# Kernel tuning notes

Hardware: AMD Instinct MI355X
Metric: run time of the kernel (lower is better)

## Reference

```python
import jax, jax.numpy as jnp
import numpy as np

B, T, C, K, NH, HID, L, NC = 16, 500, 512, 7, 8, 2048, 3, 2
HD = C // NH
SCALE = float(1.0 / np.sqrt(HD))


def setup_inputs() -> dict:
    key = jax.random.key(0)
    ks = jax.random.split(key, 24)
    rn = lambda k, sh, s=0.02: jax.random.normal(k, sh, jnp.float32) * s
    return {
        'x': jax.random.normal(ks[0], (B, T, C), jnp.float32),
        'dw_w': rn(ks[1], (L, NC, C, 1, K)),   # depthwise conv kernels (groups=C)
        'dw_b': rn(ks[2], (L, NC, C)),
        'pw_w': rn(ks[3], (L, NC, C, C)),       # pointwise 1x1 conv weights [out,in]
        'pw_b': rn(ks[4], (L, NC, C)),
        'cln_g': jnp.ones((L, NC, C), jnp.float32),
        'cln_b': jnp.zeros((L, NC, C), jnp.float32),
        'wq': rn(ks[5], (L, C, C)), 'bq': rn(ks[6], (L, C)),
        'wk': rn(ks[7], (L, C, C)), 'bk': rn(ks[8], (L, C)),
        'wv': rn(ks[9], (L, C, C)), 'bv': rn(ks[10], (L, C)),
        'wo': rn(ks[11], (L, C, C)), 'bo': rn(ks[12], (L, C)),
        'aln_g': jnp.ones((L, C), jnp.float32), 'aln_b': jnp.zeros((L, C), jnp.float32),
        'w1': rn(ks[13], (L, HID, C)), 'b1': rn(ks[14], (L, HID)),
        'w2': rn(ks[15], (L, C, HID)), 'b2': rn(ks[16], (L, C)),
        'fln_g': jnp.ones((L, C), jnp.float32), 'fln_b': jnp.zeros((L, C), jnp.float32),
    }


def _ln(x, g, b):
    m = x.mean(-1, keepdims=True)
    v = ((x - m) ** 2).mean(-1, keepdims=True)
    return (x - m) / jnp.sqrt(v + 1e-5) * g + b


def _conv_block(x, w, b, pw, pb, g, be):
    # x: (B, C, T). Depthwise conv (groups=C), padding K//2 keeps T.
    out = jax.lax.conv_general_dilated(
        x, w, window_strides=(1,), padding=[(K // 2, K // 2)],
        feature_group_count=C, dimension_numbers=('NCH', 'OIH', 'NCH')) + b[None, :, None]
    out = jnp.einsum('bct,oc->bot', out, pw) + pb[None, :, None]  # pointwise 1x1
    out = _ln(out.transpose(0, 2, 1), g, be).transpose(0, 2, 1)
    return out


def _attn(x, wq, bq, wk, bk, wv, bv, wo, bo):
    Bx, Tx, Cx = x.shape
    def split(h):
        return h.reshape(Bx, Tx, NH, HD).transpose(0, 2, 1, 3)  # (B,H,T,HD)
    q = split(x @ wq.T + bq)
    k = split(x @ wk.T + bk)
    v = split(x @ wv.T + bv)
    att = jnp.einsum('bhqd,bhkd->bhqk', q, k) * SCALE
    mask = jnp.tril(jnp.ones((Tx, Tx), bool))
    att = jnp.where(mask, att, -1e10)
    att = jax.nn.softmax(att, axis=-1)
    y = jnp.einsum('bhqk,bhkd->bhqd', att, v)
    y = y.transpose(0, 2, 1, 3).reshape(Bx, Tx, Cx)
    return y @ wo.T + bo


def _block(x, l, dw_w, dw_b, pw_w, pw_b, cln_g, cln_b, wq, bq, wk, bk, wv, bv,
           wo, bo, aln_g, aln_b, w1, b1, w2, b2, fln_g, fln_b):
    out = x.transpose(0, 2, 1)  # (B, C, T)
    for c in range(NC):
        out = _conv_block(out, dw_w[l, c], dw_b[l, c], pw_w[l, c], pw_b[l, c],
                          cln_g[l, c], cln_b[l, c])
    out = out.transpose(0, 2, 1)  # (B, T, C)
    out = _attn(out, wq[l], bq[l], wk[l], bk[l], wv[l], bv[l], wo[l], bo[l])
    out = _ln(out, aln_g[l], aln_b[l])
    out = _ln(jax.nn.relu(out @ w1[l].T + b1[l]) @ w2[l].T + b2[l], fln_g[l], fln_b[l])
    return out  # eval mode: dropouts are identity


def reference(x, dw_w, dw_b, pw_w, pw_b, cln_g, cln_b, wq, bq, wk, bk, wv, bv,
              wo, bo, aln_g, aln_b, w1, b1, w2, b2, fln_g, fln_b):
    outs = []
    h = x
    for l in range(L):
        h = _block(h, l, dw_w, dw_b, pw_w, pw_b, cln_g, cln_b, wq, bq, wk, bk,
                   wv, bv, wo, bo, aln_g, aln_b, w1, b1, w2, b2, fln_g, fln_b)
        outs.append(h)
    return tuple(outs)
```

## Files before the change

### kernel.cpp

```cpp
#include <hip/hip_runtime.h>
#include <hip/hip_bf16.h>

namespace {
constexpr int B = 16, T = 500, C = 512, KW = 7, NH = 8, HD = 64, HID = 2048;
constexpr int M = B * T;
constexpr float SCALE = 0.125f;
constexpr int BTC = B * T * C;
constexpr int CC = C * C;
constexpr int SEG_PW0 = 0;
constexpr int SEG_PW1 = CC;
constexpr int SEG_WQ  = 2 * CC;
constexpr int SEG_WK  = 3 * CC;
constexpr int SEG_WV  = 4 * CC;
constexpr int SEG_WO  = 5 * CC;
constexpr int SEG_W1  = 6 * CC;
constexpr int SEG_W2  = 6 * CC + HID * C;
constexpr int SEG_END = 6 * CC + 2 * HID * C;
}

typedef short s16x8 __attribute__((ext_vector_type(8)));
typedef float f32x4v __attribute__((ext_vector_type(4)));
typedef unsigned short u16x4 __attribute__((ext_vector_type(4)));

__device__ __forceinline__ unsigned int bfrne(float f) {
  unsigned int u = __float_as_uint(f);
  return (u + 0x7fffu + ((u >> 16) & 1u)) >> 16;
}
__device__ __forceinline__ unsigned int pack2(float a, float b) {
  return bfrne(a) | (bfrne(b) << 16);
}

__device__ __forceinline__ void gl_lds16(const unsigned short* g,
                                         unsigned short* l) {
  __builtin_amdgcn_global_load_lds(
      (const __attribute__((address_space(1))) void*)g,
      (__attribute__((address_space(3))) void*)l, 16, 0, 0);
}

__global__ __launch_bounds__(256) void cvtw_kernel(
    const float* __restrict__ pw0, const float* __restrict__ pw1,
    const float* __restrict__ wqp, const float* __restrict__ wkp,
    const float* __restrict__ wvp, const float* __restrict__ wop,
    const float* __restrict__ w1p, const float* __restrict__ w2p,
    unsigned short* __restrict__ dst) {
  size_t e = ((size_t)blockIdx.x * 256 + threadIdx.x) * 8;
  const float* src;
  size_t off;
  if      (e < SEG_PW1) { src = pw0; off = e - SEG_PW0; }
  else if (e < SEG_WQ)  { src = pw1; off = e - SEG_PW1; }
  else if (e < SEG_WK)  { src = wqp; off = e - SEG_WQ; }
  else if (e < SEG_WV)  { src = wkp; off = e - SEG_WK; }
  else if (e < SEG_WO)  { src = wvp; off = e - SEG_WV; }
  else if (e < SEG_W1)  { src = wop; off = e - SEG_WO; }
  else if (e < SEG_W2)  { src = w1p; off = e - SEG_W1; }
  else                  { src = w2p; off = e - SEG_W2; }
  float4 a = *(const float4*)(src + off);
  float4 b = *(const float4*)(src + off + 4);
  uint4 o;
  o.x = pack2(a.x, a.y); o.y = pack2(a.z, a.w);
  o.z = pack2(b.x, b.y); o.w = pack2(b.z, b.w);
  *(uint4*)(dst + e) = o;
}

__global__ __launch_bounds__(256) void biascat_kernel(
    const float* __restrict__ bq, const float* __restrict__ bk,
    const float* __restrict__ bv, float* __restrict__ dst) {
  int i = blockIdx.x * 256 + threadIdx.x;
  float v = (i < 512) ? bq[i] : (i < 1024 ? bk[i - 512] : bv[i - 1024]);
  dst[i] = v;
}

template <bool RELU, bool YBF>
__global__ __launch_bounds__(512) void gemm_mfma(
    const unsigned short* __restrict__ Xb,
    const unsigned short* __restrict__ Wb, const float* __restrict__ bias,
    void* __restrict__ Yv, int N, int K) {
  __shared__ unsigned short As[3][128 * 32];
  __shared__ unsigned short Bs[3][128 * 32];
  const int tid = threadIdx.x;
  const int w = tid >> 6, lane = tid & 63;
  const int quad = lane >> 4, r15 = lane & 15;

  const int gx = gridDim.x;
  const int nwg = gx * gridDim.y;
  const int orig = blockIdx.y * gx + blockIdx.x;
  const int q8 = nwg >> 3, r8 = nwg & 7;
  const int xcd = orig & 7, sidx = orig >> 3;
  const int tile =
      (xcd < r8 ? xcd * (q8 + 1) : r8 * (q8 + 1) + (xcd - r8) * q8) + sidx;
  const int n0 = (tile % gx) * 128;
  const int m0 = (tile / gx) * 128;

  const int srow = lane >> 2;
  const int gch = ((lane & 3) ^ (srow & 3)) * 8;
  const size_t xsrc = (size_t)min(m0 + w * 16 + srow, M - 1) * K + gch;
  const size_t wsrc = (size_t)(n0 + w * 16 + srow) * K + gch;

  auto issue = [&](int buf, int k0) {
    gl_lds16(Xb + xsrc + k0, &As[buf][w * 512]);
    gl_lds16(Wb + wsrc + k0, &Bs[buf][w * 512]);
  };

  const int wm = w >> 1, wn = w & 1;
  const int mh = wm * 32, nh = wn * 64;
  const int c0 = (quad ^ (r15 & 3)) * 8;

  f32x4v acc[2][4];
#pragma unroll
  for (int i = 0; i < 2; ++i)
#pragma unroll
    for (int j = 0; j < 4; ++j) acc[i][j] = {0.f, 0.f, 0.f, 0.f};

  const int nk = K / 32;
  issue(0, 0);
  issue(1, 32);
  int cur = 0, nxt = 2;
  for (int c = 0; c < nk; ++c) {
    if (c + 1 < nk)
      asm volatile("s_waitcnt vmcnt(2)" ::: "memory");
    else
      asm volatile("s_waitcnt vmcnt(0)" ::: "memory");
    __builtin_amdgcn_s_barrier();
    __builtin_amdgcn_sched_barrier(0);
    if (c + 2 < nk) issue(nxt, (c + 2) * 32);
    const unsigned short* Ac = As[cur];
    const unsigned short* Bc = Bs[cur];
    s16x8 af[2], bg[4];
#pragma unroll
    for (int im = 0; im < 2; ++im)
      af[im] = *(const s16x8*)&Ac[(mh + im * 16 + r15) * 32 + c0];
#pragma unroll
    for (int in = 0; in < 4; ++in)
      bg[in] = *(const s16x8*)&Bc[(nh + in * 16 + r15) * 32 + c0];
#pragma unroll
    for (int in = 0; in < 4; ++in)
#pragma unroll
      for (int im = 0; im < 2; ++im)
        acc[im][in] = __builtin_amdgcn_mfma_f32_16x16x32_bf16(
            af[im], bg[in], acc[im][in], 0, 0, 0);
    cur = (cur == 2) ? 0 : cur + 1;
    nxt = (nxt == 2) ? 0 : nxt + 1;
  }
#pragma unroll
  for (int in = 0; in < 4; ++in) {
    int col = n0 + nh + in * 16 + r15;
    float bv = bias[col];
#pragma unroll
    for (int im = 0; im < 2; ++im) {
      int rowb = m0 + mh + im * 16 + quad * 4;
#pragma unroll
      for (int r = 0; r < 4; ++r) {
        int row = rowb + r;
        if (row < M) {
          float v = acc[im][in][r] + bv;
          if (RELU) v = fmaxf(v, 0.f);
          if (YBF)
            ((unsigned short*)Yv)[(size_t)row * N + col] =
                (unsigned short)bfrne(v);
          else
            ((float*)Yv)[(size_t)row * N + col] = v;
        }
      }
    }
  }
}

__global__ __launch_bounds__(256) void dwconv_kernel(
    const float* __restrict__ X, const float* __restrict__ W,
    const float* __restrict__ bias, unsigned short* __restrict__ Y) {
  int gid = blockIdx.x * 256 + threadIdx.x;
  int b = blockIdx.y;
  int e = gid * 2;
  int t = e >> 9;
  int c = e & 511;
  float acc0 = bias[c], acc1 = bias[c + 1];
  size_t base = (size_t)b * T * C;
#pragma unroll
  for (int k = 0; k < KW; ++k) {
    int tt = t + k - 3;
    if (tt >= 0 && tt < T) {
      float2 xv = *(const float2*)&X[base + (size_t)tt * C + c];
      acc0 += xv.x * W[c * KW + k];
      acc1 += xv.y * W[(c + 1) * KW + k];
    }
  }
  *(unsigned int*)&Y[base + e] = pack2(acc0, acc1);
}

template <bool DUAL>
__global__ __launch_bounds__(256) void ln_kernel(
    const float* __restrict__ X, const float* __restrict__ g,
    const float* __restrict__ bta, float* __restrict__ Y,
    unsigned short* __restrict__ Yb) {
  int row = blockIdx.x * 4 + (threadIdx.x >> 6);
  int lane = threadIdx.x & 63;
  const float* x = X + (size_t)row * C + lane * 8;
  float4 a = *(const float4*)x;
  float4 b2 = *(const float4*)(x + 4);
  float v[8] = {a.x, a.y, a.z, a.w, b2.x, b2.y, b2.z, b2.w};
  float s = 0.f, ss = 0.f;
#pragma unroll
  for (int i = 0; i < 8; ++i) {
    s += v[i];
    ss += v[i] * v[i];
  }
#pragma unroll
  for (int off = 32; off; off >>= 1) {
    s += __shfl_xor(s, off);
    ss += __shfl_xor(ss, off);
  }
  float mean = s * (1.f / C);
  float var = ss * (1.f / C) - mean * mean;
  var = fmaxf(var, 0.f);
  float rstd = rsqrtf(var + 1e-5f);
  float4 g0 = *(const float4*)(g + lane * 8);
  float4 g1 = *(const float4*)(g + lane * 8 + 4);
  float4 be0 = *(const float4*)(bta + lane * 8);
  float4 be1 = *(const float4*)(bta + lane * 8 + 4);
  float gg[8] = {g0.x, g0.y, g0.z, g0.w, g1.x, g1.y, g1.z, g1.w};
  float bb[8] = {be0.x, be0.y, be0.z, be0.w, be1.x, be1.y, be1.z, be1.w};
  float o[8];
#pragma unroll
  for (int i = 0; i < 8; ++i) o[i] = (v[i] - mean) * rstd * gg[i] + bb[i];
  float* y = Y + (size_t)row * C + lane * 8;
  float4 w0 = {o[0], o[1], o[2], o[3]};
  float4 w1 = {o[4], o[5], o[6], o[7]};
  *(float4*)y = w0;
  *(float4*)(y + 4) = w1;
  if (DUAL) {
    uint4 ob;
    ob.x = pack2(o[0], o[1]); ob.y = pack2(o[2], o[3]);
    ob.z = pack2(o[4], o[5]); ob.w = pack2(o[6], o[7]);
    *(uint4*)(Yb + (size_t)row * C + lane * 8) = ob;
  }
}

__global__ __launch_bounds__(256) void attn_mfma_kernel(
    const unsigned short* __restrict__ QKV, unsigned short* __restrict__ Yb) {
  constexpr int QS = 3 * C;
  constexpr int LDK = 72;
  __shared__ __align__(16) unsigned short Ks[64 * LDK];
  __shared__ __align__(16) unsigned short Vt[64 * LDK];
  __shared__ __align__(16) unsigned short Ps[4][16 * LDK];
  const int tid = threadIdx.x;
  const int lane = tid & 63, w = tid >> 6;
  const int quad = lane >> 4, r15 = lane & 15;
  const int qt = blockIdx.x, hh = blockIdx.y, b = blockIdx.z;
  const int q0 = qt * 64;
  const size_t hbase = (size_t)hh * HD;

  s16x8 qa[2];
  {
    int qr = min(q0 + w * 16 + r15, T - 1);
    const unsigned short* qp = QKV + ((size_t)b * T + qr) * QS + hbase;
#pragma unroll
    for (int ks = 0; ks < 2; ++ks)
      qa[ks] = *(const s16x8*)(qp + ks * 32 + quad * 8);
  }

  f32x4v oacc[4];
  float mm[4], ll[4];
#pragma unroll
  for (int i = 0; i < 4; ++i) {
    oacc[i] = {0.f, 0.f, 0.f, 0.f};
    mm[i] = -1e30f;
    ll[i] = 0.f;
  }

  const int krow = tid >> 2, kd = (tid & 3) * 16;
  const int vk4 = (tid >> 4) * 4, vd4 = (tid & 15) * 4;

  const int kend = min(q0 + 63, T - 1);
  for (int key0 = 0; key0 <= kend; key0 += 64) {
    __syncthreads();
    {
      int key = key0 + krow;
      if (key < T) {
        const unsigned short* kp =
            QKV + ((size_t)b * T + key) * QS + C + hbase + kd;
        uint4 k0 = *(const uint4*)kp;
        uint4 k1 = *(const uint4*)(kp + 8);
        *(uint4*)&Ks[krow * LDK + kd] = k0;
        *(uint4*)&Ks[krow * LDK + kd + 8] = k1;
      } else {
        uint4 z = {0u, 0u, 0u, 0u};
        *(uint4*)&Ks[krow * LDK + kd] = z;
        *(uint4*)&Ks[krow * LDK + kd + 8] = z;
      }
    }
    {
      u16x4 va[4];
#pragma unroll
      for (int j = 0; j < 4; ++j) {
        int key = key0 + vk4 + j;
        if (key < T) {
          va[j] = *(const u16x4*)(QKV + ((size_t)b * T + key) * QS + 2 * C +
                                  hbase + vd4);
        } else {
          va[j] = (u16x4){0, 0, 0, 0};
        }
      }
#pragma unroll
      for (int i = 0; i < 4; ++i) {
        uint2 o2;
        o2.x = (unsigned int)va[0][i] | ((unsigned int)va[1][i] << 16);
        o2.y = (unsigned int)va[2][i] | ((unsigned int)va[3][i] << 16);
        *(uint2*)&Vt[(vd4 + i) * LDK + vk4] = o2;
      }
    }
    __syncthreads();

    f32x4v sa[4];
#pragma unroll
    for (int nt = 0; nt < 4; ++nt) {
      s16x8 kb0 = *(const s16x8*)&Ks[(nt * 16 + r15) * LDK + quad * 8];
      s16x8 kb1 = *(const s16x8*)&Ks[(nt * 16 + r15) * LDK + 32 + quad * 8];
      f32x4v z = {0.f, 0.f, 0.f, 0.f};
      z = __builtin_amdgcn_mfma_f32_16x16x32_bf16(qa[0], kb0, z, 0, 0, 0);
      z = __builtin_amdgcn_mfma_f32_16x16x32_bf16(qa[1], kb1, z, 0, 0, 0);
      sa[nt] = z;
    }
    const bool diag = (key0 == q0);

#pragma unroll
    for (int r = 0; r < 4; ++r) {
      int q = q0 + w * 16 + quad * 4 + r;
      float sv[4];
#pragma unroll
      for (int nt = 0; nt < 4; ++nt) {
        sv[nt] = sa[nt][r] * SCALE;
        if (diag && (key0 + nt * 16 + r15 > q)) sv[nt] = -1e30f;
      }
      float mx = fmaxf(fmaxf(sv[0], sv[1]), fmaxf(sv[2], sv[3]));
      mx = fmaxf(mx, __shfl_xor(mx, 8));
      mx = fmaxf(mx, __shfl_xor(mx, 4));
      mx = fmaxf(mx, __shfl_xor(mx, 2));
      mx = fmaxf(mx, __shfl_xor(mx, 1));
      float mnew = fmaxf(mm[r], mx);
      float alpha = __expf(mm[r] - mnew);
      float ps = 0.f;
#pragma unroll
      for (int nt = 0; nt < 4; ++nt) {
        float p = __expf(sv[nt] - mnew);
        ps += p;
        Ps[w][(quad * 4 + r) * LDK + nt * 16 + r15] =
            (unsigned short)bfrne(p);
      }
      ps += __shfl_xor(ps, 8);
      ps += __shfl_xor(ps, 4);
      ps += __shfl_xor(ps, 2);
      ps += __shfl_xor(ps, 1);
      ll[r] = ll[r] * alpha + ps;
      mm[r] = mnew;
#pragma unroll
      for (int dt = 0; dt < 4; ++dt) oacc[dt][r] *= alpha;
    }
    asm volatile("s_waitcnt lgkmcnt(0)" ::: "memory");
    __builtin_amdgcn_sched_barrier(0);

    s16x8 pa0 = *(const s16x8*)&Ps[w][r15 * LDK + quad * 8];
    s16x8 pa1 = *(const s16x8*)&Ps[w][r15 * LDK + 32 + quad * 8];
#pragma unroll
    for (int dt = 0; dt < 4; ++dt) {
      s16x8 vb0 = *(const s16x8*)&Vt[(dt * 16 + r15) * LDK + quad * 8];
      s16x8 vb1 = *(const s16x8*)&Vt[(dt * 16 + r15) * LDK + 32 + quad * 8];
      oacc[dt] =
          __builtin_amdgcn_mfma_f32_16x16x32_bf16(pa0, vb0, oacc[dt], 0, 0, 0);
      oacc[dt] =
          __builtin_amdgcn_mfma_f32_16x16x32_bf16(pa1, vb1, oacc[dt], 0, 0, 0);
    }
  }

#pragma unroll
  for (int r = 0; r < 4; ++r) {
    int q = q0 + w * 16 + quad * 4 + r;
    if (q < T) {
      float inv = 1.f / ll[r];
      unsigned short* yp = Yb + ((size_t)b * T + q) * C + hbase;
#pragma unroll
      for (int dt = 0; dt < 4; ++dt)
        yp[dt * 16 + r15] = (unsigned short)bfrne(oacc[dt][r] * inv);
    }
  }
}

extern "C" void kernel_launch(void* const* d_in, const int* in_sizes, int n_in,
                              void* d_out, int out_size, void* d_ws,
                              size_t ws_size, hipStream_t stream) {
  const float* x     = (const float*)d_in[0];
  const float* dw_w  = (const float*)d_in[1];
  const float* dw_b  = (const float*)d_in[2];
  const float* pw_w  = (const float*)d_in[3];
  const float* pw_b  = (const float*)d_in[4];
  const float* cln_g = (const float*)d_in[5];
  const float* cln_b = (const float*)d_in[6];
  const float* wq    = (const float*)d_in[7];
  const float* bq    = (const float*)d_in[8];
  const float* wk    = (const float*)d_in[9];
  const float* bk    = (const float*)d_in[10];
  const float* wv    = (const float*)d_in[11];
  const float* bv    = (const float*)d_in[12];
  const float* wo    = (const float*)d_in[13];
  const float* bo    = (const float*)d_in[14];
  const float* aln_g = (const float*)d_in[15];
  const float* aln_b = (const float*)d_in[16];
  const float* w1    = (const float*)d_in[17];
  const float* b1    = (const float*)d_in[18];
  const float* w2    = (const float*)d_in[19];
  const float* b2    = (const float*)d_in[20];
  const float* fln_g = (const float*)d_in[21];
  const float* fln_b = (const float*)d_in[22];

  float* ws = (float*)d_ws;
  float* A  = ws;
  float* Bf = ws + (size_t)BTC;
  float* R0 = ws + (size_t)2 * BTC;
  float* R1 = ws + (size_t)3 * BTC;
  float* R2 = ws + (size_t)4 * BTC;
  unsigned short* WA = (unsigned short*)(ws + (size_t)5 * BTC);
  float* out = (float*)d_out;

  unsigned short* xbf   = (unsigned short*)Bf;
  unsigned short* qkvbf = (unsigned short*)R0;
  unsigned short* fbf   = (unsigned short*)R2;
  unsigned short* hbf   = (unsigned short*)A;
  float* qkvb = A;

  dim3 blk(256);
  dim3 blkG(512);
  dim3 gemmC(C / 128, 63);
  dim3 gemmQKV(3 * C / 128, 63);
  dim3 gemmH(HID / 128, 63);
  dim3 convG(T * C / 512, B);
  dim3 attnG((T + 63) / 64, NH, B);
  int cvtwB = SEG_END / 2048;

  for (int l = 0; l < 3; ++l) {
    float* h = out + (size_t)l * BTC;
    const float* hin = (l == 0) ? x : out + (size_t)(l - 1) * BTC;
    cvtw_kernel<<<cvtwB, blk, 0, stream>>>(
        pw_w + (size_t)(2 * l) * CC, pw_w + (size_t)(2 * l + 1) * CC,
        wq + (size_t)l * CC, wk + (size_t)l * CC, wv + (size_t)l * CC,
        wo + (size_t)l * CC, w1 + (size_t)l * HID * C,
        w2 + (size_t)l * C * HID, WA);
    biascat_kernel<<<6, blk, 0, stream>>>(bq + (size_t)l * C,
                                          bk + (size_t)l * C,
                                          bv + (size_t)l * C, qkvb);
    for (int cb = 0; cb < 2; ++cb) {
      int lc = l * 2 + cb;
      const float* src = (cb == 0) ? hin : h;
      dwconv_kernel<<<convG, blk, 0, stream>>>(src, dw_w + (size_t)lc * C * KW,
                                               dw_b + (size_t)lc * C, xbf);
      gemm_mfma<false, false><<<gemmC, blkG, 0, stream>>>(
          xbf, WA + (cb ? SEG_PW1 : SEG_PW0), pw_b + (size_t)lc * C, R0, C, C);
      if (cb == 0)
        ln_kernel<false><<<M / 4, blk, 0, stream>>>(
            R0, cln_g + (size_t)lc * C, cln_b + (size_t)lc * C, h, nullptr);
      else
        ln_kernel<true><<<M / 4, blk, 0, stream>>>(
            R0, cln_g + (size_t)lc * C, cln_b + (size_t)lc * C, h, xbf);
    }
    gemm_mfma<false, true><<<gemmQKV, blkG, 0, stream>>>(
        xbf, WA + SEG_WQ, qkvb, qkvbf, 3 * C, C);
    attn_mfma_kernel<<<attnG, blk, 0, stream>>>(qkvbf, xbf);
    gemm_mfma<false, false><<<gemmC, blkG, 0, stream>>>(
        xbf, WA + SEG_WO, bo + (size_t)l * C, R1, C, C);
    ln_kernel<true><<<M / 4, blk, 0, stream>>>(
        R1, aln_g + (size_t)l * C, aln_b + (size_t)l * C, h, fbf);
    gemm_mfma<true, true><<<gemmH, blkG, 0, stream>>>(
        fbf, WA + SEG_W1, b1 + (size_t)l * HID, hbf, HID, C);
    gemm_mfma<false, false><<<gemmC, blkG, 0, stream>>>(
        hbf, WA + SEG_W2, b2 + (size_t)l * C, R0, C, HID);
    ln_kernel<false><<<M / 4, blk, 0, stream>>>(
        R0, fln_g + (size_t)l * C, fln_b + (size_t)l * C, h, nullptr);
  }
}
```

Baseline: 1.046 ms.

## Split-K the N=512 GEMMs in two and sum the partials inside LayerNorm

The N=512 GEMMs (pointwise conv, output projection, FFN down) launch with a K-split of two along grid z, giving 504 workgroups instead of 252 on a 256-CU device. Each half writes its own fp32 partial buffer, and the following LayerNorm kernel adds the two partials as it loads them, so no separate reduction kernel is needed. The LDS swizzle for loads and fragment reads also changes to XOR with bits 1-2 of the row instead of bits 0-1, which changes the bank-conflict pattern. In exchange the GEMMs write twice as much fp32 output and LayerNorm reads twice as much, and R0 must now hold two BTC-sized slices.

```diff
diff --git a/kernel.cpp b/kernel.cpp
--- a/kernel.cpp
+++ b/kernel.cpp
@@ -70,7 +70,7 @@
   dst[i] = v;
 }
 
-template <bool RELU, bool YBF>
+template <bool RELU, bool YBF, bool SPLIT>
 __global__ __launch_bounds__(512) void gemm_mfma(
     const unsigned short* __restrict__ Xb,
     const unsigned short* __restrict__ Wb, const float* __restrict__ bias,
@@ -81,6 +81,10 @@
   const int w = tid >> 6, lane = tid & 63;
   const int quad = lane >> 4, r15 = lane & 15;
 
+  const int ks = SPLIT ? blockIdx.z : 0;
+  const int K2 = SPLIT ? (K >> 1) : K;
+  const int kbase = ks * K2;
+
   const int gx = gridDim.x;
   const int nwg = gx * gridDim.y;
   const int orig = blockIdx.y * gx + blockIdx.x;
@@ -92,9 +96,10 @@
   const int m0 = (tile / gx) * 128;
 
   const int srow = lane >> 2;
-  const int gch = ((lane & 3) ^ (srow & 3)) * 8;
-  const size_t xsrc = (size_t)min(m0 + w * 16 + srow, M - 1) * K + gch;
-  const size_t wsrc = (size_t)(n0 + w * 16 + srow) * K + gch;
+  const int gch = ((lane & 3) ^ ((lane >> 3) & 3)) * 8;
+  const size_t xsrc =
+      (size_t)min(m0 + w * 16 + srow, M - 1) * K + kbase + gch;
+  const size_t wsrc = (size_t)(n0 + w * 16 + srow) * K + kbase + gch;
 
   auto issue = [&](int buf, int k0) {
     gl_lds16(Xb + xsrc + k0, &As[buf][w * 512]);
@@ -103,7 +108,7 @@
 
   const int wm = w >> 1, wn = w & 1;
   const int mh = wm * 32, nh = wn * 64;
-  const int c0 = (quad ^ (r15 & 3)) * 8;
+  const int c0 = (quad ^ ((r15 >> 1) & 3)) * 8;
 
   f32x4v acc[2][4];
 #pragma unroll
@@ -111,7 +116,7 @@
 #pragma unroll
     for (int j = 0; j < 4; ++j) acc[i][j] = {0.f, 0.f, 0.f, 0.f};
 
-  const int nk = K / 32;
+  const int nk = K2 / 32;
   issue(0, 0);
   issue(1, 32);
   int cur = 0, nxt = 2;
@@ -141,10 +146,12 @@
     cur = (cur == 2) ? 0 : cur + 1;
     nxt = (nxt == 2) ? 0 : nxt + 1;
   }
+  float* Yf = (float*)Yv + (SPLIT ? (size_t)ks * M * N : 0);
 #pragma unroll
   for (int in = 0; in < 4; ++in) {
     int col = n0 + nh + in * 16 + r15;
     float bv = bias[col];
+    if (SPLIT && ks) bv = 0.f;
 #pragma unroll
     for (int im = 0; im < 2; ++im) {
       int rowb = m0 + mh + im * 16 + quad * 4;
@@ -158,7 +165,7 @@
             ((unsigned short*)Yv)[(size_t)row * N + col] =
                 (unsigned short)bfrne(v);
           else
-            ((float*)Yv)[(size_t)row * N + col] = v;
+            Yf[(size_t)row * N + col] = v;
         }
       }
     }
@@ -187,7 +194,7 @@
   *(unsigned int*)&Y[base + e] = pack2(acc0, acc1);
 }
 
-template <bool DUAL>
+template <bool DUAL, bool SUM2>
 __global__ __launch_bounds__(256) void ln_kernel(
     const float* __restrict__ X, const float* __restrict__ g,
     const float* __restrict__ bta, float* __restrict__ Y,
@@ -198,6 +205,13 @@
   float4 a = *(const float4*)x;
   float4 b2 = *(const float4*)(x + 4);
   float v[8] = {a.x, a.y, a.z, a.w, b2.x, b2.y, b2.z, b2.w};
+  if (SUM2) {
+    const float* x2 = x + (size_t)BTC;
+    float4 a2 = *(const float4*)x2;
+    float4 b3 = *(const float4*)(x2 + 4);
+    v[0] += a2.x; v[1] += a2.y; v[2] += a2.z; v[3] += a2.w;
+    v[4] += b3.x; v[5] += b3.y; v[6] += b3.z; v[7] += b3.w;
+  }
   float s = 0.f, ss = 0.f;
 #pragma unroll
   for (int i = 0; i < 8; ++i) {
@@ -428,7 +442,7 @@
 
   dim3 blk(256);
   dim3 blkG(512);
-  dim3 gemmC(C / 128, 63);
+  dim3 gemmC2(C / 128, 63, 2);
   dim3 gemmQKV(3 * C / 128, 63);
   dim3 gemmH(HID / 128, 63);
   dim3 convG(T * C / 512, B);
@@ -451,27 +465,27 @@
       const float* src = (cb == 0) ? hin : h;
       dwconv_kernel<<<convG, blk, 0, stream>>>(src, dw_w + (size_t)lc * C * KW,
                                                dw_b + (size_t)lc * C, xbf);
-      gemm_mfma<false, false><<<gemmC, blkG, 0, stream>>>(
+      gemm_mfma<false, false, true><<<gemmC2, blkG, 0, stream>>>(
           xbf, WA + (cb ? SEG_PW1 : SEG_PW0), pw_b + (size_t)lc * C, R0, C, C);
       if (cb == 0)
-        ln_kernel<false><<<M / 4, blk, 0, stream>>>(
+        ln_kernel<false, true><<<M / 4, blk, 0, stream>>>(
             R0, cln_g + (size_t)lc * C, cln_b + (size_t)lc * C, h, nullptr);
       else
-        ln_kernel<true><<<M / 4, blk, 0, stream>>>(
+        ln_kernel<true, true><<<M / 4, blk, 0, stream>>>(
             R0, cln_g + (size_t)lc * C, cln_b + (size_t)lc * C, h, xbf);
     }
-    gemm_mfma<false, true><<<gemmQKV, blkG, 0, stream>>>(
+    gemm_mfma<false, true, false><<<gemmQKV, blkG, 0, stream>>>(
         xbf, WA + SEG_WQ, qkvb, qkvbf, 3 * C, C);
     attn_mfma_kernel<<<attnG, blk, 0, stream>>>(qkvbf, xbf);
-    gemm_mfma<false, false><<<gemmC, blkG, 0, stream>>>(
-        xbf, WA + SEG_WO, bo + (size_t)l * C, R1, C, C);
-    ln_kernel<true><<<M / 4, blk, 0, stream>>>(
-        R1, aln_g + (size_t)l * C, aln_b + (size_t)l * C, h, fbf);
-    gemm_mfma<true, true><<<gemmH, blkG, 0, stream>>>(
+    gemm_mfma<false, false, true><<<gemmC2, blkG, 0, stream>>>(
+        xbf, WA + SEG_WO, bo + (size_t)l * C, R0, C, C);
+    ln_kernel<true, true><<<M / 4, blk, 0, stream>>>(
+        R0, aln_g + (size_t)l * C, aln_b + (size_t)l * C, h, fbf);
+    gemm_mfma<true, true, false><<<gemmH, blkG, 0, stream>>>(
         fbf, WA + SEG_W1, b1 + (size_t)l * HID, hbf, HID, C);
-    gemm_mfma<false, false><<<gemmC, blkG, 0, stream>>>(
+    gemm_mfma<false, false, true><<<gemmC2, blkG, 0, stream>>>(
         hbf, WA + SEG_W2, b2 + (size_t)l * C, R0, C, HID);
-    ln_kernel<false><<<M / 4, blk, 0, stream>>>(
+    ln_kernel<false, true><<<M / 4, blk, 0, stream>>>(
         R0, fln_g + (size_t)l * C, fln_b + (size_t)l * C, h, nullptr);
   }
 }
```

Measured after the change: 977.6 us. -6.5%, faster.
